# Optimization experiments

Hardware: AMD Instinct MI355X
Metric: run time of the kernel (lower is better)

The kernel has to match this reference:

```python
import jax, jax.numpy as jnp
import numpy as np

T = 200000


def _sine_layer(tvec, A, w, phi, phic, wc):
    # tvec: (t,), A/w/phi: (n,1), phic/wc: (1,)
    phi_static = jax.nn.relu(phic)  # (1,)
    w_static = jax.nn.relu(wc)
    ph = jax.nn.relu(phi) + phi_static  # (n,1)
    ww = jax.nn.relu(w) + w_static
    sine = A * jnp.sin(ww * tvec[None, :] + ph)  # (n,t)
    return sine, phi_static, w_static


def _selector_layer(tvec, wave_input, w, phi, phic, wc, phi_prev, w_prev):
    # wave_input: (n,t), w/phi: (m,n), phic/wc/phi_prev/w_prev: (1,)
    # NOTE: phi_prev/w_prev passed but phi_prev flag is False in the network,
    # so they are NOT added (matches torch: `if self.phi_prev and ...`).
    phi_static = jax.nn.relu(phic)
    w_static = jax.nn.relu(wc)
    ph = (jax.nn.relu(phi) + phi_static)[:, :, None]  # (m,n,1)
    ww = (jax.nn.relu(w) + w_static)[:, :, None]
    sine = 0.5 * jnp.sin(ww * tvec[None, None, :] + ph) + 0.5  # (m,n,t)
    out = jnp.einsum('mnt,nt->mt', sine, wave_input)  # (m,t)
    return out, phi_static, w_static


def setup_inputs() -> dict:
    key = jax.random.key(0)
    ks = jax.random.split(key, 18)
    r = lambda k, s: jax.random.normal(k, s, dtype=jnp.float32)
    return {
        'initial_wave_input': r(ks[0], (20, T)),
        'A0': r(ks[1], (20, 1)), 'w0': r(ks[2], (20, 1)), 'phi0': r(ks[3], (20, 1)),
        'wc0': r(ks[4], (1,)), 'phic0': r(ks[5], (1,)),
        'w1': r(ks[6], (25, 20)), 'phi1': r(ks[7], (25, 20)),
        'wc1': r(ks[8], (1,)), 'phic1': r(ks[9], (1,)),
        'w2': r(ks[10], (30, 25)), 'phi2': r(ks[11], (30, 25)),
        'wc2': r(ks[12], (1,)), 'phic2': r(ks[13], (1,)),
        'w3': r(ks[14], (1, 30)), 'phi3': r(ks[15], (1, 30)),
        'wc3': r(ks[16], (1,)), 'phic3': r(ks[17], (1,)),
    }


def reference(initial_wave_input, A0, w0, phi0, wc0, phic0,
              w1, phi1, wc1, phic1, w2, phi2, wc2, phic2,
              w3, phi3, wc3, phic3):
    tvec = jnp.linspace(1.0, 1000.0, T, dtype=jnp.float32)
    # initial_wave_input is an argument of the torch module but is never used.
    s, phi, w = _sine_layer(tvec, A0, w0, phi0, phic0, wc0)
    s, phi, w = _selector_layer(tvec, s, w1, phi1, phic1, wc1, phi, w)
    s, phi, w = _selector_layer(tvec, s, w2, phi2, phic2, wc2, phi, w)
    s, phi, w = _selector_layer(tvec, s, w3, phi3, phic3, wc3, phi, w)
    return s  # (1, t)
```

## Files before the change

kernel.cpp:

```cpp
#include <hip/hip_runtime.h>
#include <hip/hip_bf16.h>

#define T_TOTAL 200000
#define NTILE   782
#define STEPF   (999.0f / 199999.0f)

typedef float v4f __attribute__((ext_vector_type(4)));

__device__ float g_P[5200];
__device__ float g_s1[NTILE * 6400];

__device__ __forceinline__ float sinp(float rev) {
    float g = __builtin_amdgcn_fractf(rev);
    float h = g - 0.5f;
    float u = h * h;
    float p = fmaf(45.621248f, u, -82.391040f);
    p = fmaf(p, u, 64.671616f);
    p = fmaf(p, u, -19.730960f);
    p = fmaf(p, u, 0.9999618f);
    return p;
}

__global__ void prep_kernel(
    const float* __restrict__ A0,
    const float* __restrict__ w0, const float* __restrict__ phi0,
    const float* __restrict__ wc0, const float* __restrict__ phic0,
    const float* __restrict__ w1, const float* __restrict__ phi1,
    const float* __restrict__ wc1, const float* __restrict__ phic1,
    const float* __restrict__ w2, const float* __restrict__ phi2,
    const float* __restrict__ wc2, const float* __restrict__ phic2,
    const float* __restrict__ w3, const float* __restrict__ phi3,
    const float* __restrict__ wc3, const float* __restrict__ phic3)
{
    const int tid = blockIdx.x * blockDim.x + threadIdx.x;
    const int stride = blockDim.x * gridDim.x;

    const double I2PI = 0.15915494309189535;
    const double D1   = 999.0 / 199999.0;

    const double ws0 = fmax((double)wc0[0], 0.0), ps0 = fmax((double)phic0[0], 0.0);
    const double ws1 = fmax((double)wc1[0], 0.0), ps1 = fmax((double)phic1[0], 0.0);
    const double ws2 = fmax((double)wc2[0], 0.0), ps2 = fmax((double)phic2[0], 0.0);
    const double ws3 = fmax((double)wc3[0], 0.0), ps3 = fmax((double)phic3[0], 0.0);

    for (int n = tid; n < 20; n += stride) {
        double wr = fmax((double)w0[n], 0.0) + ws0;
        g_P[4 * n]     = (float)(wr * I2PI);
        g_P[4 * n + 1] = (float)((fmax((double)phi0[n], 0.0) + ps0) * I2PI + 0.25);
        g_P[4 * n + 2] = (float)(2.0 * cos(wr * D1));
        g_P[4 * n + 3] = A0[n];
    }
    for (int k = tid; k < 25 * 20; k += stride) {
        double wr = fmax((double)w1[k], 0.0) + ws1;
        g_P[80 + 4 * k]     = (float)(wr * I2PI);
        g_P[80 + 4 * k + 1] = (float)((fmax((double)phi1[k], 0.0) + ps1) * I2PI + 0.25);
        g_P[80 + 4 * k + 2] = (float)(2.0 * cos(wr * D1));
        g_P[80 + 4 * k + 3] = 0.0f;
    }
    for (int k = tid; k < 30 * 25; k += stride) {
        double wr = fmax((double)w2[k], 0.0) + ws2;
        g_P[2080 + 4 * k]     = (float)(wr * I2PI);
        g_P[2080 + 4 * k + 1] = (float)((fmax((double)phi2[k], 0.0) + ps2) * I2PI + 0.25);
        g_P[2080 + 4 * k + 2] = (float)(2.0 * cos(wr * D1));
        g_P[2080 + 4 * k + 3] = 0.0f;
    }
    for (int m = tid; m < 30; m += stride) {
        double wr = fmax((double)w3[m], 0.0) + ws3;
        g_P[5080 + 4 * m]     = (float)(wr * I2PI);
        g_P[5080 + 4 * m + 1] = (float)((fmax((double)phi3[m], 0.0) + ps3) * I2PI + 0.25);
        g_P[5080 + 4 * m + 2] = (float)(2.0 * cos(wr * D1));
        g_P[5080 + 4 * m + 3] = 0.0f;
    }
}

__launch_bounds__(256)
__global__ void k_l01()
{
    __shared__ float pp[2000];
    __shared__ float s0s[20 * 256];

    const int tid = threadIdx.x;
    for (int i = tid; i < 2000; i += 256) pp[i] = g_P[80 + i];

    const int l = tid & 63;
    const int w = __builtin_amdgcn_readfirstlane(tid >> 6);
    const int tb = blockIdx.x * 256;
    const int tl = 4 * l;
    const float tv0 = fmaf((float)(tb + tl), STEPF, 1.0f);
    const float tv1 = tv0 + STEPF;

#pragma unroll
    for (int i = 0; i < 5; ++i) {
        const int n = 5 * w + i;
        const v4f q = *(const v4f*)&g_P[4 * n];
        float x0 = q[3] * sinp(fmaf(q[0], tv0, q[1]));
        float x1 = q[3] * sinp(fmaf(q[0], tv1, q[1]));
        float x2 = fmaf(q[2], x1, -x0);
        float x3 = fmaf(q[2], x2, -x1);
        *(v4f*)&s0s[n * 256 + tl] = (v4f){x0, x1, x2, x3};
    }
    __syncthreads();

    float sum0[4] = {0.f, 0.f, 0.f, 0.f};
#pragma unroll
    for (int n = 0; n < 20; ++n) {
        const v4f s = *(const v4f*)&s0s[n * 256 + tl];
        sum0[0] += s[0]; sum0[1] += s[1]; sum0[2] += s[2]; sum0[3] += s[3];
    }

    const int mS = w ? (1 + 6 * w) : 0;
    const int mC = w ? 6 : 7;
    for (int i = 0; i < mC; ++i) {
        const int m = mS + i;
        const float* __restrict__ pb = &pp[80 * m];
        float a0 = 0.f, a1 = 0.f, a2 = 0.f, a3 = 0.f;
#pragma unroll
        for (int n = 0; n < 20; ++n) {
            const v4f q = *(const v4f*)&pb[4 * n];
            const v4f s = *(const v4f*)&s0s[n * 256 + tl];
            float x0 = sinp(fmaf(q[0], tv0, q[1]));
            float x1 = sinp(fmaf(q[0], tv1, q[1]));
            float x2 = fmaf(q[2], x1, -x0);
            float x3 = fmaf(q[2], x2, -x1);
            a0 = fmaf(x0, s[0], a0);
            a1 = fmaf(x1, s[1], a1);
            a2 = fmaf(x2, s[2], a2);
            a3 = fmaf(x3, s[3], a3);
        }
        const v4f o = {fmaf(0.5f, a0, 0.5f * sum0[0]),
                       fmaf(0.5f, a1, 0.5f * sum0[1]),
                       fmaf(0.5f, a2, 0.5f * sum0[2]),
                       fmaf(0.5f, a3, 0.5f * sum0[3])};
        *(v4f*)&g_s1[blockIdx.x * 6400 + m * 256 + tl] = o;
    }
}

__launch_bounds__(256)
__global__ void k_l23(float* __restrict__ out)
{
    __shared__ float pp[3120];
    __shared__ float s1s[25 * 256];
    __shared__ float shp[4 * 256];

    const int tid = threadIdx.x;
    const int tb = blockIdx.x * 256;

    {
        const v4f* __restrict__ src = (const v4f*)&g_s1[blockIdx.x * 6400];
        v4f* __restrict__ dst = (v4f*)s1s;
        for (int i = tid; i < 1600; i += 256) dst[i] = src[i];
    }
    for (int i = tid; i < 3120; i += 256) pp[i] = g_P[2080 + i];
    __syncthreads();

    const int l = tid & 63;
    const int w = __builtin_amdgcn_readfirstlane(tid >> 6);
    const int tl = 4 * l;
    const float tv0 = fmaf((float)(tb + tl), STEPF, 1.0f);
    const float tv1 = tv0 + STEPF;

    float sum1[4] = {0.f, 0.f, 0.f, 0.f};
#pragma unroll
    for (int n = 0; n < 25; ++n) {
        const v4f s = *(const v4f*)&s1s[n * 256 + tl];
        sum1[0] += s[0]; sum1[1] += s[1]; sum1[2] += s[2]; sum1[3] += s[3];
    }

    const int mS = (w < 2) ? 8 * w : (16 + 7 * (w - 2));
    const int mC = (w < 2) ? 8 : 7;
    float pw0 = 0.f, pw1 = 0.f, pw2 = 0.f, pw3 = 0.f;
    for (int i = 0; i < mC; ++i) {
        const int m = mS + i;
        const float* __restrict__ pb = &pp[100 * m];
        float a0 = 0.f, a1 = 0.f, a2 = 0.f, a3 = 0.f;
#pragma unroll
        for (int n = 0; n < 25; ++n) {
            const v4f q = *(const v4f*)&pb[4 * n];
            const v4f s = *(const v4f*)&s1s[n * 256 + tl];
            float x0 = sinp(fmaf(q[0], tv0, q[1]));
            float x1 = sinp(fmaf(q[0], tv1, q[1]));
            float x2 = fmaf(q[2], x1, -x0);
            float x3 = fmaf(q[2], x2, -x1);
            a0 = fmaf(x0, s[0], a0);
            a1 = fmaf(x1, s[1], a1);
            a2 = fmaf(x2, s[2], a2);
            a3 = fmaf(x3, s[3], a3);
        }
        const v4f q3 = *(const v4f*)&pp[3000 + 4 * m];
        float y0 = sinp(fmaf(q3[0], tv0, q3[1]));
        float y1 = sinp(fmaf(q3[0], tv1, q3[1]));
        float y2 = fmaf(q3[2], y1, -y0);
        float y3 = fmaf(q3[2], y2, -y1);
        pw0 = fmaf(fmaf(0.5f, y0, 0.5f), fmaf(0.5f, a0, 0.5f * sum1[0]), pw0);
        pw1 = fmaf(fmaf(0.5f, y1, 0.5f), fmaf(0.5f, a1, 0.5f * sum1[1]), pw1);
        pw2 = fmaf(fmaf(0.5f, y2, 0.5f), fmaf(0.5f, a2, 0.5f * sum1[2]), pw2);
        pw3 = fmaf(fmaf(0.5f, y3, 0.5f), fmaf(0.5f, a3, 0.5f * sum1[3]), pw3);
    }
    *(v4f*)&shp[w * 256 + tl] = (v4f){pw0, pw1, pw2, pw3};
    __syncthreads();

    const int tlr = 64 * w + l;
    const float r = (shp[tlr] + shp[256 + tlr]) + (shp[512 + tlr] + shp[768 + tlr]);
    const int tt = tb + tlr;
    if (tt < T_TOTAL) out[tt] = r;
}

extern "C" void kernel_launch(void* const* d_in, const int* in_sizes, int n_in,
                              void* d_out, int out_size, void* d_ws, size_t ws_size,
                              hipStream_t stream) {
    (void)in_sizes; (void)n_in; (void)d_ws; (void)ws_size; (void)out_size;
    const float* A0    = (const float*)d_in[1];
    const float* w0    = (const float*)d_in[2];
    const float* phi0  = (const float*)d_in[3];
    const float* wc0   = (const float*)d_in[4];
    const float* phic0 = (const float*)d_in[5];
    const float* w1    = (const float*)d_in[6];
    const float* phi1  = (const float*)d_in[7];
    const float* wc1   = (const float*)d_in[8];
    const float* phic1 = (const float*)d_in[9];
    const float* w2    = (const float*)d_in[10];
    const float* phi2  = (const float*)d_in[11];
    const float* wc2   = (const float*)d_in[12];
    const float* phic2 = (const float*)d_in[13];
    const float* w3    = (const float*)d_in[14];
    const float* phi3  = (const float*)d_in[15];
    const float* wc3   = (const float*)d_in[16];
    const float* phic3 = (const float*)d_in[17];

    float* out = (float*)d_out;

    hipLaunchKernelGGL(prep_kernel, dim3(6), dim3(256), 0, stream,
                       A0, w0, phi0, wc0, phic0,
                       w1, phi1, wc1, phic1,
                       w2, phi2, wc2, phic2,
                       w3, phi3, wc3, phic3);

    hipLaunchKernelGGL(k_l01, dim3(NTILE), dim3(256), 0, stream);
    hipLaunchKernelGGL(k_l23, dim3(NTILE), dim3(256), 0, stream, out);
}
```

Measured before the change: 58.48 us.

## Split layer-2/3 work across two blocks per tile with a combine kernel

Measured after the change: 73.58 us. 1.26x slower.

```diff
diff --git a/kernel.cpp b/kernel.cpp
--- a/kernel.cpp
+++ b/kernel.cpp
@@ -9,6 +9,7 @@
 
 __device__ float g_P[5200];
 __device__ float g_s1[NTILE * 6400];
+__device__ float g_part[2 * NTILE * 256];
 
 __device__ __forceinline__ float sinp(float rev) {
     float g = __builtin_amdgcn_fractf(rev);
@@ -136,21 +137,24 @@
 }
 
 __launch_bounds__(256)
-__global__ void k_l23(float* __restrict__ out)
-{
-    __shared__ float pp[3120];
+__global__ void k_l23()
+{
     __shared__ float s1s[25 * 256];
-    __shared__ float shp[4 * 256];
+    __shared__ float pp[1560];
 
     const int tid = threadIdx.x;
-    const int tb = blockIdx.x * 256;
+    const int h = blockIdx.x & 1;
+    const int tile = blockIdx.x >> 1;
+    const int tb = tile * 256;
 
     {
-        const v4f* __restrict__ src = (const v4f*)&g_s1[blockIdx.x * 6400];
+        const v4f* __restrict__ src = (const v4f*)&g_s1[tile * 6400];
         v4f* __restrict__ dst = (v4f*)s1s;
         for (int i = tid; i < 1600; i += 256) dst[i] = src[i];
     }
-    for (int i = tid; i < 3120; i += 256) pp[i] = g_P[2080 + i];
+    for (int i = tid; i < 1560; i += 256)
+        pp[i] = (i < 1500) ? g_P[2080 + 1500 * h + i]
+                           : g_P[5080 + 60 * h + (i - 1500)];
     __syncthreads();
 
     const int l = tid & 63;
@@ -166,8 +170,8 @@
         sum1[0] += s[0]; sum1[1] += s[1]; sum1[2] += s[2]; sum1[3] += s[3];
     }
 
-    const int mS = (w < 2) ? 8 * w : (16 + 7 * (w - 2));
-    const int mC = (w < 2) ? 8 : 7;
+    const int mS = 4 * w;
+    const int mC = (w == 3) ? 3 : 4;
     float pw0 = 0.f, pw1 = 0.f, pw2 = 0.f, pw3 = 0.f;
     for (int i = 0; i < mC; ++i) {
         const int m = mS + i;
@@ -186,7 +190,7 @@
             a2 = fmaf(x2, s[2], a2);
             a3 = fmaf(x3, s[3], a3);
         }
-        const v4f q3 = *(const v4f*)&pp[3000 + 4 * m];
+        const v4f q3 = *(const v4f*)&pp[1500 + 4 * m];
         float y0 = sinp(fmaf(q3[0], tv0, q3[1]));
         float y1 = sinp(fmaf(q3[0], tv1, q3[1]));
         float y2 = fmaf(q3[2], y1, -y0);
@@ -196,13 +200,21 @@
         pw2 = fmaf(fmaf(0.5f, y2, 0.5f), fmaf(0.5f, a2, 0.5f * sum1[2]), pw2);
         pw3 = fmaf(fmaf(0.5f, y3, 0.5f), fmaf(0.5f, a3, 0.5f * sum1[3]), pw3);
     }
+    __syncthreads();
+    float* const shp = s1s;
     *(v4f*)&shp[w * 256 + tl] = (v4f){pw0, pw1, pw2, pw3};
     __syncthreads();
 
     const int tlr = 64 * w + l;
     const float r = (shp[tlr] + shp[256 + tlr]) + (shp[512 + tlr] + shp[768 + tlr]);
-    const int tt = tb + tlr;
-    if (tt < T_TOTAL) out[tt] = r;
+    g_part[h * (NTILE * 256) + tb + tlr] = r;
+}
+
+__launch_bounds__(256)
+__global__ void k_comb(float* __restrict__ out)
+{
+    const int t = blockIdx.x * 256 + threadIdx.x;
+    if (t < T_TOTAL) out[t] = g_part[t] + g_part[NTILE * 256 + t];
 }
 
 extern "C" void kernel_launch(void* const* d_in, const int* in_sizes, int n_in,
@@ -236,5 +248,6 @@
                        w3, phi3, wc3, phic3);
 
     hipLaunchKernelGGL(k_l01, dim3(NTILE), dim3(256), 0, stream);
-    hipLaunchKernelGGL(k_l23, dim3(NTILE), dim3(256), 0, stream, out);
-}
+    hipLaunchKernelGGL(k_l23, dim3(2 * NTILE), dim3(256), 0, stream);
+    hipLaunchKernelGGL(k_comb, dim3(NTILE), dim3(256), 0, stream, out);
+}
```
